# Kernel tuning notes

Measured on AMD Instinct MI355X. Metric: run time of the kernel, lower is better.

The kernel has to match this reference:

```python
import jax, jax.numpy as jnp
import numpy as np

D_OUT, D_IN, RANK = 4096, 4096, 512
BATCH, SEQ = 4, 2048


def setup_inputs() -> dict:
    key = jax.random.key(0)
    kx, ka, kb, kc = jax.random.split(key, 4)
    x = jax.random.normal(kx, (BATCH, SEQ, D_IN), dtype=jnp.float32)
    # CP/low-rank factors: weight = A @ B.T, shape [D_OUT, D_IN]
    A = jax.random.normal(ka, (D_OUT, RANK), dtype=jnp.float32) * (1.0 / np.sqrt(RANK))
    B = jax.random.normal(kb, (D_IN, RANK), dtype=jnp.float32) * (1.0 / np.sqrt(D_IN))
    bias = jax.random.normal(kc, (D_OUT,), dtype=jnp.float32)
    return {"x": x, "A": A, "B": B, "bias": bias}


def reference(x, A, B, bias):
    # method == 'cp_2d': reconstruct weight then apply F.linear
    weight = A @ B.T                      # [D_OUT, D_IN]
    # F.linear(x, W, b) = x @ W.T + b
    out = jnp.einsum('bsd,od->bso', x, weight) + bias
    return out
```

## Files before the change

kernel.cpp:

```cpp
#include <hip/hip_runtime.h>

typedef __attribute__((ext_vector_type(8))) __bf16 bf16x8;
typedef __attribute__((ext_vector_type(4))) __bf16 bf16x4;
typedef __attribute__((ext_vector_type(4))) float f32x4;

#define D_OUT 4096
#define D_IN  4096
#define RANK  512
#define MROWS 8192

__device__ __forceinline__ void gload_lds16(const void* gsrc, void* ldst) {
  __builtin_amdgcn_global_load_lds(
      (const __attribute__((address_space(1))) void*)gsrc,
      (__attribute__((address_space(3))) void*)ldst, 16, 0, 0);
}

__global__ __launch_bounds__(256) void cvt_f32_bf16(const float* __restrict__ in,
                                                    __bf16* __restrict__ out,
                                                    size_t n) {
  size_t i = ((size_t)blockIdx.x * 256 + threadIdx.x) * 4;
  size_t stride = (size_t)gridDim.x * 256 * 4;
  for (; i < n; i += stride) {
    float4 v = *(const float4*)(in + i);
    bf16x4 o = {(__bf16)v.x, (__bf16)v.y, (__bf16)v.z, (__bf16)v.w};
    *(bf16x4*)(out + i) = o;
  }
}

__global__ __launch_bounds__(256) void transpose_cvt(const float* __restrict__ in,
                                                     __bf16* __restrict__ out,
                                                     int R, int C) {
  __shared__ __bf16 tile[64][72];
  const int r0 = blockIdx.x * 64, c0 = blockIdx.y * 64;
  const int t = threadIdx.x;
  const int tr = t / 16, tc4 = (t % 16) * 4;
#pragma unroll
  for (int i = 0; i < 4; ++i) {
    int r = i * 16 + tr;
    float4 v = *(const float4*)(in + (size_t)(r0 + r) * C + c0 + tc4);
    tile[r][tc4 + 0] = (__bf16)v.x;
    tile[r][tc4 + 1] = (__bf16)v.y;
    tile[r][tc4 + 2] = (__bf16)v.z;
    tile[r][tc4 + 3] = (__bf16)v.w;
  }
  __syncthreads();
#pragma unroll
  for (int i = 0; i < 4; ++i) {
    int c = i * 16 + tr;
    bf16x4 o = {tile[tc4 + 0][c], tile[tc4 + 1][c], tile[tc4 + 2][c], tile[tc4 + 3][c]};
    *(bf16x4*)(out + (size_t)(c0 + c) * R + r0 + tc4) = o;
  }
}

__global__ __launch_bounds__(256) void reduce2_bf16(const __bf16* __restrict__ t0,
                                                    const __bf16* __restrict__ t1,
                                                    __bf16* __restrict__ o) {
  size_t i = ((size_t)blockIdx.x * 256 + threadIdx.x) * 8;
  bf16x8 a = *(const bf16x8*)(t0 + i);
  bf16x8 b = *(const bf16x8*)(t1 + i);
  bf16x8 r;
#pragma unroll
  for (int j = 0; j < 8; ++j) r[j] = (__bf16)((float)a[j] + (float)b[j]);
  *(bf16x8*)(o + i) = r;
}

template <int BM, int BN, int BK>
__global__ __launch_bounds__(256) void gemm1_xf32(const float* __restrict__ Xf,
                                                  const __bf16* __restrict__ Bmat,
                                                  __bf16* __restrict__ Cout,
                                                  int M, int N, int Kred, int ldk) {
  constexpr int WM = BM / 2, WN = BN / 2;
  constexpr int MI = WM / 16, NI = WN / 16;
  __shared__ alignas(16) float Af[BM * BK];
  __shared__ alignas(16) __bf16 Bl[BN * BK];

  const int tid = threadIdx.x;
  const int wid = tid >> 6;
  const int lane = tid & 63;
  const int l15 = lane & 15, lhi = lane >> 4;
  const int wr = wid >> 1, wc = wid & 1;

  const int m0 = blockIdx.x * BM;
  const int n0 = blockIdx.y * BN;
  const int kbase = blockIdx.z * Kred;

  f32x4 acc[MI][NI] = {};

  for (int k0 = kbase; k0 < kbase + Kred; k0 += BK) {
    constexpr int IAF = BM * BK / (256 * 4);
#pragma unroll
    for (int it = 0; it < IAF; ++it) {
      int o = (it * 256 + tid) * 4;
      int row = o / BK;
      int b = (o % BK) / 4;
      int colsw = (b ^ (row & 7)) * 4;
      gload_lds16(Xf + (size_t)(m0 + row) * ldk + k0 + colsw,
                  Af + (it * 256 + wid * 64) * 4);
    }
    constexpr int IB = BN * BK / (256 * 8);
#pragma unroll
    for (int it = 0; it < IB; ++it) {
      int o = (it * 256 + tid) * 8;
      int row = o / BK;
      int blk = (o % BK) / 8;
      int col = (blk ^ (row & 7)) * 8;
      gload_lds16(Bmat + (size_t)(n0 + row) * ldk + k0 + col,
                  Bl + (it * 256 + wid * 64) * 8);
    }
    __syncthreads();

#pragma unroll
    for (int kk = 0; kk < BK / 32; ++kk) {
      bf16x8 af[MI], bfv[NI];
#pragma unroll
      for (int mi = 0; mi < MI; ++mi) {
        int row = wr * WM + mi * 16 + l15;
        int b0 = (kk * 8 + lhi * 2) ^ (row & 7);
        const char* base = (const char*)Af + row * (BK * 4);
        f32x4 a0 = *(const f32x4*)(base + b0 * 16);
        f32x4 a1 = *(const f32x4*)(base + (b0 ^ 1) * 16);
#pragma unroll
        for (int j = 0; j < 4; ++j) {
          af[mi][j]     = (__bf16)a0[j];
          af[mi][4 + j] = (__bf16)a1[j];
        }
      }
#pragma unroll
      for (int ni = 0; ni < NI; ++ni) {
        int row = wc * WN + ni * 16 + l15;
        int blk = (kk * 4 + lhi) ^ (row & 7);
        bfv[ni] = *(const bf16x8*)((const char*)Bl + row * (BK * 2) + blk * 16);
      }
#pragma unroll
      for (int mi = 0; mi < MI; ++mi)
#pragma unroll
        for (int ni = 0; ni < NI; ++ni)
          acc[mi][ni] = __builtin_amdgcn_mfma_f32_16x16x32_bf16(af[mi], bfv[ni],
                                                                acc[mi][ni], 0, 0, 0);
    }
    __syncthreads();
  }

  __bf16* cbase = Cout + (size_t)blockIdx.z * M * N;
#pragma unroll
  for (int ni = 0; ni < NI; ++ni) {
    int col = n0 + wc * WN + ni * 16 + l15;
#pragma unroll
    for (int mi = 0; mi < MI; ++mi) {
#pragma unroll
      for (int r = 0; r < 4; ++r) {
        int row = m0 + wr * WM + mi * 16 + lhi * 4 + r;
        cbase[(size_t)row * N + col] = (__bf16)acc[mi][ni][r];
      }
    }
  }
}

template <int BM, int BN, int BK>
__global__ __launch_bounds__(256) void gemm_bt_bias(const __bf16* __restrict__ Amat,
                                                    const __bf16* __restrict__ Bmat,
                                                    const float* __restrict__ bias,
                                                    float* __restrict__ Cout,
                                                    int M, int N, int K) {
  constexpr int WM = BM / 2, WN = BN / 2;
  constexpr int MI = WM / 16, NI = WN / 16;
  __shared__ alignas(16) __bf16 Al[BM * BK];
  __shared__ alignas(16) __bf16 Bl[BN * BK];

  const int tid = threadIdx.x;
  const int wid = tid >> 6;
  const int lane = tid & 63;
  const int l15 = lane & 15, lhi = lane >> 4;
  const int wr = wid >> 1, wc = wid & 1;

  const int m0 = blockIdx.x * BM;
  const int n0 = blockIdx.y * BN;

  f32x4 acc[MI][NI] = {};

  for (int k0 = 0; k0 < K; k0 += BK) {
    constexpr int IA = BM * BK / (256 * 8);
#pragma unroll
    for (int it = 0; it < IA; ++it) {
      int o = (it * 256 + tid) * 8;
      int row = o / BK;
      int blk = (o % BK) / 8;
      int col = (blk ^ (row & 7)) * 8;
      gload_lds16(Amat + (size_t)(m0 + row) * K + k0 + col,
                  Al + (it * 256 + wid * 64) * 8);
    }
    constexpr int IB = BN * BK / (256 * 8);
#pragma unroll
    for (int it = 0; it < IB; ++it) {
      int o = (it * 256 + tid) * 8;
      int row = o / BK;
      int blk = (o % BK) / 8;
      int col = (blk ^ (row & 7)) * 8;
      gload_lds16(Bmat + (size_t)(n0 + row) * K + k0 + col,
                  Bl + (it * 256 + wid * 64) * 8);
    }
    __syncthreads();

#pragma unroll
    for (int kk = 0; kk < BK / 32; ++kk) {
      bf16x8 af[MI], bfv[NI];
#pragma unroll
      for (int mi = 0; mi < MI; ++mi) {
        int row = wr * WM + mi * 16 + l15;
        int blk = (kk * 4 + lhi) ^ (row & 7);
        af[mi] = *(const bf16x8*)((const char*)Al + row * (BK * 2) + blk * 16);
      }
#pragma unroll
      for (int ni = 0; ni < NI; ++ni) {
        int row = wc * WN + ni * 16 + l15;
        int blk = (kk * 4 + lhi) ^ (row & 7);
        bfv[ni] = *(const bf16x8*)((const char*)Bl + row * (BK * 2) + blk * 16);
      }
#pragma unroll
      for (int mi = 0; mi < MI; ++mi)
#pragma unroll
        for (int ni = 0; ni < NI; ++ni)
          acc[mi][ni] = __builtin_amdgcn_mfma_f32_16x16x32_bf16(af[mi], bfv[ni],
                                                                acc[mi][ni], 0, 0, 0);
    }
    __syncthreads();
  }

#pragma unroll
  for (int ni = 0; ni < NI; ++ni) {
    int col = n0 + wc * WN + ni * 16 + l15;
    float bv = bias[col];
#pragma unroll
    for (int mi = 0; mi < MI; ++mi) {
#pragma unroll
      for (int r = 0; r < 4; ++r) {
        int row = m0 + wr * WM + mi * 16 + lhi * 4 + r;
        Cout[(size_t)row * N + col] = acc[mi][ni][r] + bv;
      }
    }
  }
}

extern "C" void kernel_launch(void* const* d_in, const int* in_sizes, int n_in,
                              void* d_out, int out_size, void* d_ws, size_t ws_size,
                              hipStream_t stream) {
  const float* x    = (const float*)d_in[0];
  const float* A    = (const float*)d_in[1];
  const float* B    = (const float*)d_in[2];
  const float* bias = (const float*)d_in[3];
  float* out = (float*)d_out;

  __bf16* tp = (__bf16*)((char*)d_out + ((size_t)64 << 20));
  char* ws = (char*)d_ws;
  __bf16* Ab = (__bf16*)ws;
  __bf16* Bt = (__bf16*)(ws + ((size_t)4 << 20));
  __bf16* Tt = (__bf16*)(ws + ((size_t)8 << 20));

  hipLaunchKernelGGL(cvt_f32_bf16, dim3(512), dim3(256), 0, stream,
                     A, Ab, (size_t)D_OUT * RANK);
  hipLaunchKernelGGL(transpose_cvt, dim3(D_IN / 64, RANK / 64), dim3(256), 0, stream,
                     B, Bt, D_IN, RANK);
  hipLaunchKernelGGL((gemm1_xf32<128, 128, 64>),
                     dim3(MROWS / 128, RANK / 128, 2), dim3(256), 0, stream,
                     x, Bt, tp, MROWS, RANK, D_IN / 2, D_IN);
  hipLaunchKernelGGL(reduce2_bf16, dim3(MROWS * RANK / (256 * 8)), dim3(256), 0, stream,
                     tp, tp + (size_t)MROWS * RANK, Tt);
  hipLaunchKernelGGL((gemm_bt_bias<128, 128, 64>),
                     dim3(MROWS / 128, D_OUT / 128), dim3(256), 0, stream,
                     Tt, Ab, bias, out, MROWS, D_OUT, RANK);
}
```

Before: 141.2 us.

## Double-buffer LDS tiles in both GEMMs with async prefetch two stages ahead

Both GEMM kernels are rewritten to use two LDS buffers with BK=32. The next-next tile is issued via global_load_lds while the current tile's MFMAs run, and explicit vmcnt waits and barriers replace the full syncthreads pairs. The LDS swizzle is adjusted for the 64-byte bf16 rows. This is meant to hide global load latency behind compute, at the cost of more barriers per K and a smaller K step per iteration.

```diff
diff --git a/kernel.cpp b/kernel.cpp
--- a/kernel.cpp
+++ b/kernel.cpp
@@ -64,15 +64,14 @@
   *(bf16x8*)(o + i) = r;
 }
 
-template <int BM, int BN, int BK>
-__global__ __launch_bounds__(256) void gemm1_xf32(const float* __restrict__ Xf,
+__global__ __launch_bounds__(256) void gemm1_pipe(const float* __restrict__ Xf,
                                                   const __bf16* __restrict__ Bmat,
                                                   __bf16* __restrict__ Cout,
                                                   int M, int N, int Kred, int ldk) {
-  constexpr int WM = BM / 2, WN = BN / 2;
-  constexpr int MI = WM / 16, NI = WN / 16;
-  __shared__ alignas(16) float Af[BM * BK];
-  __shared__ alignas(16) __bf16 Bl[BN * BK];
+  constexpr int BM = 128, BN = 128, BK = 32;
+  constexpr int MI = 4, NI = 4;
+  __shared__ alignas(16) float  Af[2][BM * BK];
+  __shared__ alignas(16) __bf16 Bl[2][BN * BK];
 
   const int tid = threadIdx.x;
   const int wid = tid >> 6;
@@ -83,89 +82,106 @@
   const int m0 = blockIdx.x * BM;
   const int n0 = blockIdx.y * BN;
   const int kbase = blockIdx.z * Kred;
+  const int nt = Kred / BK;
 
   f32x4 acc[MI][NI] = {};
 
-  for (int k0 = kbase; k0 < kbase + Kred; k0 += BK) {
-    constexpr int IAF = BM * BK / (256 * 4);
-#pragma unroll
-    for (int it = 0; it < IAF; ++it) {
+  auto stage = [&](int t, int c) {
+    const int k0 = kbase + t * BK;
+#pragma unroll
+    for (int it = 0; it < 4; ++it) {
       int o = (it * 256 + tid) * 4;
-      int row = o / BK;
-      int b = (o % BK) / 4;
+      int row = o >> 5;
+      int b = (o & 31) >> 2;
       int colsw = (b ^ (row & 7)) * 4;
       gload_lds16(Xf + (size_t)(m0 + row) * ldk + k0 + colsw,
-                  Af + (it * 256 + wid * 64) * 4);
-    }
-    constexpr int IB = BN * BK / (256 * 8);
-#pragma unroll
-    for (int it = 0; it < IB; ++it) {
+                  &Af[c][(it * 256 + wid * 64) * 4]);
+    }
+#pragma unroll
+    for (int it = 0; it < 2; ++it) {
       int o = (it * 256 + tid) * 8;
-      int row = o / BK;
-      int blk = (o % BK) / 8;
-      int col = (blk ^ (row & 7)) * 8;
-      gload_lds16(Bmat + (size_t)(n0 + row) * ldk + k0 + col,
-                  Bl + (it * 256 + wid * 64) * 8);
-    }
-    __syncthreads();
-
-#pragma unroll
-    for (int kk = 0; kk < BK / 32; ++kk) {
-      bf16x8 af[MI], bfv[NI];
-#pragma unroll
-      for (int mi = 0; mi < MI; ++mi) {
-        int row = wr * WM + mi * 16 + l15;
-        int b0 = (kk * 8 + lhi * 2) ^ (row & 7);
-        const char* base = (const char*)Af + row * (BK * 4);
-        f32x4 a0 = *(const f32x4*)(base + b0 * 16);
-        f32x4 a1 = *(const f32x4*)(base + (b0 ^ 1) * 16);
-#pragma unroll
-        for (int j = 0; j < 4; ++j) {
-          af[mi][j]     = (__bf16)a0[j];
-          af[mi][4 + j] = (__bf16)a1[j];
-        }
+      int row = o >> 5;
+      int b = (o & 31) >> 3;
+      int colsw = (b ^ ((row >> 1) & 3)) * 8;
+      gload_lds16(Bmat + (size_t)(n0 + row) * ldk + k0 + colsw,
+                  &Bl[c][(it * 256 + wid * 64) * 8]);
+    }
+  };
+
+  stage(0, 0);
+  stage(1, 1);
+  asm volatile("s_waitcnt vmcnt(6)" ::: "memory");
+  __builtin_amdgcn_s_barrier();
+
+  for (int t = 0; t < nt; ++t) {
+    const int c = t & 1;
+    bf16x8 af[MI];
+    bf16x8 bfv[NI];
+#pragma unroll
+    for (int mi = 0; mi < MI; ++mi) {
+      int row = wr * 64 + mi * 16 + l15;
+      int p0 = (lhi * 2) ^ (row & 7);
+      const char* base = (const char*)&Af[c][0] + row * 128;
+      f32x4 a0 = *(const f32x4*)(base + p0 * 16);
+      f32x4 a1 = *(const f32x4*)(base + (p0 ^ 1) * 16);
+#pragma unroll
+      for (int j = 0; j < 4; ++j) {
+        af[mi][j]     = (__bf16)a0[j];
+        af[mi][4 + j] = (__bf16)a1[j];
       }
-#pragma unroll
-      for (int ni = 0; ni < NI; ++ni) {
-        int row = wc * WN + ni * 16 + l15;
-        int blk = (kk * 4 + lhi) ^ (row & 7);
-        bfv[ni] = *(const bf16x8*)((const char*)Bl + row * (BK * 2) + blk * 16);
-      }
-#pragma unroll
-      for (int mi = 0; mi < MI; ++mi)
-#pragma unroll
-        for (int ni = 0; ni < NI; ++ni)
-          acc[mi][ni] = __builtin_amdgcn_mfma_f32_16x16x32_bf16(af[mi], bfv[ni],
-                                                                acc[mi][ni], 0, 0, 0);
-    }
-    __syncthreads();
+    }
+#pragma unroll
+    for (int ni = 0; ni < NI; ++ni) {
+      int row = wc * 64 + ni * 16 + l15;
+      int p = lhi ^ ((row >> 1) & 3);
+      bfv[ni] = *(const bf16x8*)((const char*)&Bl[c][0] + row * 64 + p * 16);
+    }
+    asm volatile("s_waitcnt lgkmcnt(0)" ::: "memory");
+    __builtin_amdgcn_sched_barrier(0);
+    __builtin_amdgcn_s_barrier();
+
+    if (t + 2 < nt) stage(t + 2, c);
+
+#pragma unroll
+    for (int mi = 0; mi < MI; ++mi)
+#pragma unroll
+      for (int ni = 0; ni < NI; ++ni)
+        acc[mi][ni] = __builtin_amdgcn_mfma_f32_16x16x32_bf16(af[mi], bfv[ni],
+                                                              acc[mi][ni], 0, 0, 0);
+
+    if (t + 1 < nt) {
+      if (t + 2 < nt)
+        asm volatile("s_waitcnt vmcnt(6)" ::: "memory");
+      else
+        asm volatile("s_waitcnt vmcnt(0)" ::: "memory");
+      __builtin_amdgcn_s_barrier();
+    }
   }
 
   __bf16* cbase = Cout + (size_t)blockIdx.z * M * N;
 #pragma unroll
   for (int ni = 0; ni < NI; ++ni) {
-    int col = n0 + wc * WN + ni * 16 + l15;
+    int col = n0 + wc * 64 + ni * 16 + l15;
 #pragma unroll
     for (int mi = 0; mi < MI; ++mi) {
 #pragma unroll
       for (int r = 0; r < 4; ++r) {
-        int row = m0 + wr * WM + mi * 16 + lhi * 4 + r;
+        int row = m0 + wr * 64 + mi * 16 + lhi * 4 + r;
         cbase[(size_t)row * N + col] = (__bf16)acc[mi][ni][r];
       }
     }
   }
 }
 
-template <int BM, int BN, int BK>
-__global__ __launch_bounds__(256) void gemm_bt_bias(const __bf16* __restrict__ Amat,
-                                                    const __bf16* __restrict__ Bmat,
-                                                    const float* __restrict__ bias,
-                                                    float* __restrict__ Cout,
-                                                    int M, int N, int K) {
-  constexpr int WM = BM / 2, WN = BN / 2;
-  constexpr int MI = WM / 16, NI = WN / 16;
-  __shared__ alignas(16) __bf16 Al[BM * BK];
-  __shared__ alignas(16) __bf16 Bl[BN * BK];
+__global__ __launch_bounds__(256) void gemm2_pipe(const __bf16* __restrict__ Amat,
+                                                  const __bf16* __restrict__ Bmat,
+                                                  const float* __restrict__ bias,
+                                                  float* __restrict__ Cout,
+                                                  int M, int N, int K) {
+  constexpr int BM = 128, BN = 128, BK = 32;
+  constexpr int MI = 4, NI = 4;
+  __shared__ alignas(16) __bf16 Al[2][BM * BK];
+  __shared__ alignas(16) __bf16 Bl[2][BN * BK];
 
   const int tid = threadIdx.x;
   const int wid = tid >> 6;
@@ -175,66 +191,84 @@
 
   const int m0 = blockIdx.x * BM;
   const int n0 = blockIdx.y * BN;
+  const int nt = K / BK;
 
   f32x4 acc[MI][NI] = {};
 
-  for (int k0 = 0; k0 < K; k0 += BK) {
-    constexpr int IA = BM * BK / (256 * 8);
-#pragma unroll
-    for (int it = 0; it < IA; ++it) {
+  auto stage = [&](int t, int c) {
+    const int k0 = t * BK;
+#pragma unroll
+    for (int it = 0; it < 2; ++it) {
       int o = (it * 256 + tid) * 8;
-      int row = o / BK;
-      int blk = (o % BK) / 8;
-      int col = (blk ^ (row & 7)) * 8;
-      gload_lds16(Amat + (size_t)(m0 + row) * K + k0 + col,
-                  Al + (it * 256 + wid * 64) * 8);
-    }
-    constexpr int IB = BN * BK / (256 * 8);
-#pragma unroll
-    for (int it = 0; it < IB; ++it) {
+      int row = o >> 5;
+      int b = (o & 31) >> 3;
+      int colsw = (b ^ ((row >> 1) & 3)) * 8;
+      gload_lds16(Amat + (size_t)(m0 + row) * K + k0 + colsw,
+                  &Al[c][(it * 256 + wid * 64) * 8]);
+    }
+#pragma unroll
+    for (int it = 0; it < 2; ++it) {
       int o = (it * 256 + tid) * 8;
-      int row = o / BK;
-      int blk = (o % BK) / 8;
-      int col = (blk ^ (row & 7)) * 8;
-      gload_lds16(Bmat + (size_t)(n0 + row) * K + k0 + col,
-                  Bl + (it * 256 + wid * 64) * 8);
-    }
-    __syncthreads();
-
-#pragma unroll
-    for (int kk = 0; kk < BK / 32; ++kk) {
-      bf16x8 af[MI], bfv[NI];
-#pragma unroll
-      for (int mi = 0; mi < MI; ++mi) {
-        int row = wr * WM + mi * 16 + l15;
-        int blk = (kk * 4 + lhi) ^ (row & 7);
-        af[mi] = *(const bf16x8*)((const char*)Al + row * (BK * 2) + blk * 16);
-      }
-#pragma unroll
-      for (int ni = 0; ni < NI; ++ni) {
-        int row = wc * WN + ni * 16 + l15;
-        int blk = (kk * 4 + lhi) ^ (row & 7);
-        bfv[ni] = *(const bf16x8*)((const char*)Bl + row * (BK * 2) + blk * 16);
-      }
-#pragma unroll
-      for (int mi = 0; mi < MI; ++mi)
-#pragma unroll
-        for (int ni = 0; ni < NI; ++ni)
-          acc[mi][ni] = __builtin_amdgcn_mfma_f32_16x16x32_bf16(af[mi], bfv[ni],
-                                                                acc[mi][ni], 0, 0, 0);
-    }
-    __syncthreads();
+      int row = o >> 5;
+      int b = (o & 31) >> 3;
+      int colsw = (b ^ ((row >> 1) & 3)) * 8;
+      gload_lds16(Bmat + (size_t)(n0 + row) * K + k0 + colsw,
+                  &Bl[c][(it * 256 + wid * 64) * 8]);
+    }
+  };
+
+  stage(0, 0);
+  stage(1, 1);
+  asm volatile("s_waitcnt vmcnt(4)" ::: "memory");
+  __builtin_amdgcn_s_barrier();
+
+  for (int t = 0; t < nt; ++t) {
+    const int c = t & 1;
+    bf16x8 af[MI];
+    bf16x8 bfv[NI];
+#pragma unroll
+    for (int mi = 0; mi < MI; ++mi) {
+      int row = wr * 64 + mi * 16 + l15;
+      int p = lhi ^ ((row >> 1) & 3);
+      af[mi] = *(const bf16x8*)((const char*)&Al[c][0] + row * 64 + p * 16);
+    }
+#pragma unroll
+    for (int ni = 0; ni < NI; ++ni) {
+      int row = wc * 64 + ni * 16 + l15;
+      int p = lhi ^ ((row >> 1) & 3);
+      bfv[ni] = *(const bf16x8*)((const char*)&Bl[c][0] + row * 64 + p * 16);
+    }
+    asm volatile("s_waitcnt lgkmcnt(0)" ::: "memory");
+    __builtin_amdgcn_sched_barrier(0);
+    __builtin_amdgcn_s_barrier();
+
+    if (t + 2 < nt) stage(t + 2, c);
+
+#pragma unroll
+    for (int mi = 0; mi < MI; ++mi)
+#pragma unroll
+      for (int ni = 0; ni < NI; ++ni)
+        acc[mi][ni] = __builtin_amdgcn_mfma_f32_16x16x32_bf16(af[mi], bfv[ni],
+                                                              acc[mi][ni], 0, 0, 0);
+
+    if (t + 1 < nt) {
+      if (t + 2 < nt)
+        asm volatile("s_waitcnt vmcnt(4)" ::: "memory");
+      else
+        asm volatile("s_waitcnt vmcnt(0)" ::: "memory");
+      __builtin_amdgcn_s_barrier();
+    }
   }
 
 #pragma unroll
   for (int ni = 0; ni < NI; ++ni) {
-    int col = n0 + wc * WN + ni * 16 + l15;
+    int col = n0 + wc * 64 + ni * 16 + l15;
     float bv = bias[col];
 #pragma unroll
     for (int mi = 0; mi < MI; ++mi) {
 #pragma unroll
       for (int r = 0; r < 4; ++r) {
-        int row = m0 + wr * WM + mi * 16 + lhi * 4 + r;
+        int row = m0 + wr * 64 + mi * 16 + lhi * 4 + r;
         Cout[(size_t)row * N + col] = acc[mi][ni][r] + bv;
       }
     }
@@ -260,12 +294,12 @@
                      A, Ab, (size_t)D_OUT * RANK);
   hipLaunchKernelGGL(transpose_cvt, dim3(D_IN / 64, RANK / 64), dim3(256), 0, stream,
                      B, Bt, D_IN, RANK);
-  hipLaunchKernelGGL((gemm1_xf32<128, 128, 64>),
+  hipLaunchKernelGGL(gemm1_pipe,
                      dim3(MROWS / 128, RANK / 128, 2), dim3(256), 0, stream,
                      x, Bt, tp, MROWS, RANK, D_IN / 2, D_IN);
   hipLaunchKernelGGL(reduce2_bf16, dim3(MROWS * RANK / (256 * 8)), dim3(256), 0, stream,
                      tp, tp + (size_t)MROWS * RANK, Tt);
-  hipLaunchKernelGGL((gemm_bt_bias<128, 128, 64>),
+  hipLaunchKernelGGL(gemm2_pipe,
                      dim3(MROWS / 128, D_OUT / 128), dim3(256), 0, stream,
                      Tt, Ab, bias, out, MROWS, D_OUT, RANK);
 }
```

New measurement: 154.1 us. 1.09x slower.
